# Performance work log

Measured on AMD Instinct MI355X. Metric: run time of the kernel, lower is better.

The kernel has to match this reference:

```python
import jax, jax.numpy as jnp
import numpy as np

B, S_SRC, S_TGT = 32, 128, 128
V, E, H = 32000, 256, 256
PAD_ID = 0
NEG = -1.0e9


def setup_inputs() -> dict:
    key = jax.random.key(0)
    ks = jax.random.split(key, 16)
    lengths_de = jax.random.randint(ks[0], (B,), S_SRC // 2, S_SRC + 1)
    idx_de = jax.random.randint(ks[1], (B, S_SRC), 1, V)
    pos = jnp.arange(S_SRC)[None, :]
    indices_de = jnp.where(pos < lengths_de[:, None], idx_de, PAD_ID)
    indices_en = jax.random.randint(ks[2], (B, S_TGT), 1, V)
    lengths_en = jnp.full((B,), S_TGT, dtype=jnp.int32)

    sc = 0.02
    def nrm(k, shape):
        return jax.random.normal(k, shape, dtype=jnp.float32) * sc
    emb_enc = nrm(ks[3], (V, E)).at[PAD_ID].set(0.0)
    emb_dec = nrm(ks[4], (V, E)).at[PAD_ID].set(0.0)
    return {
        "indices_de": indices_de, "lengths_de": lengths_de,
        "indices_en": indices_en, "lengths_en": lengths_en,
        "emb_enc": emb_enc, "emb_dec": emb_dec,
        "W_ih_enc": nrm(ks[5], (H, E)), "W_hh_enc": nrm(ks[6], (H, H)),
        "b_ih_enc": jnp.zeros((H,), jnp.float32), "b_hh_enc": jnp.zeros((H,), jnp.float32),
        "W_ih_dec": nrm(ks[7], (H, E)), "W_hh_dec": nrm(ks[8], (H, H)),
        "b_ih_dec": jnp.zeros((H,), jnp.float32), "b_hh_dec": jnp.zeros((H,), jnp.float32),
        "W_attn": nrm(ks[9], (H, 2 * H)), "b_attn": jnp.zeros((H,), jnp.float32),
        "W_out": nrm(ks[10], (V, H)), "b_out": jnp.zeros((V,), jnp.float32),
    }


def reference(indices_de, lengths_de, indices_en, lengths_en,
              emb_enc, emb_dec,
              W_ih_enc, W_hh_enc, b_ih_enc, b_hh_enc,
              W_ih_dec, W_hh_dec, b_ih_dec, b_hh_dec,
              W_attn, b_attn, W_out, b_out):
    # ---- Encoder: tanh RNN over packed sequence ----
    x_enc = emb_enc[indices_de]                      # [B, S, E]
    valid = jnp.arange(S_SRC)[None, :] < lengths_de[:, None]  # [B, S]

    def enc_step(h, inp):
        x_t, v_t = inp                                # [B,E], [B]
        h_new = jnp.tanh(x_t @ W_ih_enc.T + b_ih_enc + h @ W_hh_enc.T + b_hh_enc)
        h = jnp.where(v_t[:, None], h_new, h)         # frozen past length (pack semantics)
        out = jnp.where(v_t[:, None], h_new, 0.0)     # padded outputs are zero
        return h, out

    h0 = jnp.zeros((B, H), jnp.float32)
    h_final, enc_outs = jax.lax.scan(
        enc_step, h0, (x_enc.transpose(1, 0, 2), valid.T))
    encoder_outputs = enc_outs.transpose(1, 0, 2)     # [B, S, H]
    enc_mask = indices_de == PAD_ID                   # [B, S] True at padding

    # ---- Decoder: per-step RNN cell + dot-product attention + vocab proj ----
    x_dec = emb_dec[indices_en]                       # [B, T, E]

    def dec_step(h, x_t):
        h = jnp.tanh(x_t @ W_ih_dec.T + b_ih_dec + h @ W_hh_dec.T + b_hh_dec)
        scores = jnp.einsum('bh,bsh->bs', h, encoder_outputs)
        scores = jnp.where(enc_mask, NEG, scores)
        attn = jax.nn.softmax(scores, axis=-1)
        context = jnp.einsum('bs,bsh->bh', attn, encoder_outputs)
        combined = jnp.concatenate([context, h], axis=1)          # [B, 2H]
        attn_out = jnp.tanh(combined @ W_attn.T + b_attn)         # [B, H]
        logits_t = attn_out @ W_out.T + b_out                     # [B, V]
        return h, logits_t

    _, logits = jax.lax.scan(dec_step, h_final, x_dec.transpose(1, 0, 2))
    return logits.transpose(1, 0, 2)                  # [B, T, V]
```

## Files before the change

### kernel.cpp

```cpp
#include <hip/hip_runtime.h>
#include <stdint.h>

#define B_ 32
#define S_ 128
#define T_ 128
#define V_ 32000
#define E_ 256
#define H_ 256
#define NEG_ (-1.0e9f)

typedef __attribute__((ext_vector_type(8))) short short8;
typedef __attribute__((ext_vector_type(4))) float floatx4;

__device__ __forceinline__ unsigned short f2bf(float x){
  unsigned u = __float_as_uint(x);
  u = u + 0x7fffu + ((u >> 16) & 1u);
  return (unsigned short)(u >> 16);
}
__device__ __forceinline__ float bf2f(unsigned short s){
  return __uint_as_float(((unsigned)s) << 16);
}
__device__ __forceinline__ float hsum4(float4 v){ return (v.x+v.y)+(v.z+v.w); }
__device__ __forceinline__ void unpack8(uint4 q, float4& lo, float4& hi){
  lo.x = __uint_as_float(q.x << 16); lo.y = __uint_as_float(q.x & 0xffff0000u);
  lo.z = __uint_as_float(q.y << 16); lo.w = __uint_as_float(q.y & 0xffff0000u);
  hi.x = __uint_as_float(q.z << 16); hi.y = __uint_as_float(q.z & 0xffff0000u);
  hi.z = __uint_as_float(q.w << 16); hi.w = __uint_as_float(q.w & 0xffff0000u);
}

__global__ void k_cvt(const float* __restrict__ src, unsigned short* __restrict__ dst, int n4){
  int i = blockIdx.x*256 + threadIdx.x;
  if (i < n4){
    float4 v = ((const float4*)src)[i];
    ushort4 o; o.x=f2bf(v.x); o.y=f2bf(v.y); o.z=f2bf(v.z); o.w=f2bf(v.w);
    ((ushort4*)dst)[i] = o;
  }
}

__global__ __launch_bounds__(256) void k_xih(
    const int* __restrict__ idxmat,
    const float* __restrict__ emb,
    const float* __restrict__ Wih,
    const float* __restrict__ b1, const float* __restrict__ b2,
    float* __restrict__ out)
{
  __shared__ int idx_s[16];
  __shared__ float4 x_s[16][64];
  int b = blockIdx.x >> 3;
  int t0 = (blockIdx.x & 7) << 4;
  int tid = threadIdx.x;
  if (tid < 16) idx_s[tid] = idxmat[b*128 + t0 + tid];
  __syncthreads();
  for (int r = 0; r < 16; ++r)
    ((float*)&x_s[r][0])[tid] = emb[(size_t)idx_s[r]*E_ + tid];
  __syncthreads();
  int j2 = tid & 127, tg = tid >> 7;
  const float4* W0 = (const float4*)(Wih + (size_t)j2*E_);
  const float4* W1 = (const float4*)(Wih + (size_t)(j2+128)*E_);
  float4 a0[8], a1[8];
  #pragma unroll
  for (int t=0;t<8;++t){ a0[t]={0,0,0,0}; a1[t]={0,0,0,0}; }
  for (int e4 = 0; e4 < 64; ++e4){
    float4 w0 = W0[e4], w1 = W1[e4];
    #pragma unroll
    for (int t = 0; t < 8; ++t){
      float4 xv = x_s[tg*8+t][e4];
      a0[t] += w0*xv; a1[t] += w1*xv;
    }
  }
  float bi0 = b1[j2] + b2[j2];
  float bi1 = b1[j2+128] + b2[j2+128];
  #pragma unroll
  for (int t = 0; t < 8; ++t){
    size_t row = (size_t)((b<<7) + t0 + tg*8 + t)*H_;
    out[row + j2]     = hsum4(a0[t]) + bi0;
    out[row + j2+128] = hsum4(a1[t]) + bi1;
  }
}

template<int ENC>
__global__ __launch_bounds__(512, 2) void k_rnn(
    const float* __restrict__ Whh,
    const float* __restrict__ Xih,
    const float* __restrict__ h0,
    const int* __restrict__ lengths,
    unsigned short* __restrict__ enc_out,
    float* __restrict__ hseq,
    float* __restrict__ hfinal)
{
  __shared__ float4 h4_s[64];
  __shared__ float part[2][256];
  float* h_s = (float*)h4_s;
  int b = blockIdx.x, tid = threadIdx.x;
  int j = tid & 255, half = tid >> 8;
  float4 w[32];
  const float4* Wr = (const float4*)(Whh + (size_t)j*H_ + half*128);
  #pragma unroll
  for (int i = 0; i < 32; ++i) w[i] = Wr[i];
  if (tid < 256) h_s[tid] = ENC ? 0.f : h0[b*H_ + tid];
  int len = ENC ? lengths[b] : T_;
  __syncthreads();
  for (int t = 0; t < 128; ++t){
    float x = 0.f;
    if (tid < 256) x = Xih[(size_t)((b<<7) + t)*H_ + j];
    const float4* hh = h4_s + (half << 5);
    float4 acc0 = {0,0,0,0}, acc1 = {0,0,0,0};
    #pragma unroll
    for (int i = 0; i < 32; i += 2){ acc0 += w[i]*hh[i]; acc1 += w[i+1]*hh[i+1]; }
    part[half][j] = hsum4(acc0) + hsum4(acc1);
    __syncthreads();
    if (tid < 256){
      float s = x + part[0][tid] + part[1][tid];
      float hn = tanhf(s);
      if (ENC){
        float hold = h_s[tid];
        bool v = (t < len);
        h_s[tid] = v ? hn : hold;
        enc_out[(size_t)((b<<7)+t)*H_ + tid] = f2bf(v ? hn : 0.f);
      } else {
        h_s[tid] = hn;
        hseq[(size_t)((b<<7)+t)*H_ + tid] = hn;
      }
    }
    __syncthreads();
  }
  if (ENC && tid < 256) hfinal[b*H_ + tid] = h_s[tid];
}

__global__ __launch_bounds__(256) void k_attn(
    const unsigned short* __restrict__ enc_out,
    const float* __restrict__ hseq,
    const int* __restrict__ lengths,
    const unsigned short* __restrict__ Wattn,
    const float* __restrict__ battn,
    unsigned short* __restrict__ attn_out)
{
  __shared__ float h_sm[16][256];
  __shared__ float sc[16][132];
  __shared__ float comb[16][512];
  int bx = blockIdx.x; int b = bx >> 3; int t0 = (bx & 7) << 4;
  int tid = threadIdx.x;
  int len = lengths[b];
  for (int r = 0; r < 16; ++r)
    h_sm[r][tid] = hseq[(size_t)((b<<7) + t0 + r)*H_ + tid];
  __syncthreads();
  {
    int s = tid & 127, tg = tid >> 7;
    float4 a[8];
    #pragma unroll
    for (int t=0;t<8;++t) a[t] = {0,0,0,0};
    const uint4* ep = (const uint4*)(enc_out + (size_t)(b*S_ + s)*H_);
    for (int oct = 0; oct < 32; ++oct){
      uint4 q = ep[oct];
      float4 elo, ehi; unpack8(q, elo, ehi);
      #pragma unroll
      for (int t = 0; t < 8; ++t){
        const float4* hp = (const float4*)&h_sm[tg*8+t][oct*8];
        a[t] += elo*hp[0] + ehi*hp[1];
      }
    }
    #pragma unroll
    for (int t = 0; t < 8; ++t)
      sc[tg*8+t][s] = (s < len) ? hsum4(a[t]) : NEG_;
  }
  __syncthreads();
  {
    int wv = tid >> 6, ln = tid & 63;
    for (int r = 0; r < 4; ++r){
      int t = r*4 + wv;
      float v0 = sc[t][ln], v1 = sc[t][ln+64];
      float m = fmaxf(v0, v1);
      #pragma unroll
      for (int off = 32; off >= 1; off >>= 1) m = fmaxf(m, __shfl_xor(m, off));
      float e0 = __expf(v0 - m), e1 = __expf(v1 - m);
      float su = e0 + e1;
      #pragma unroll
      for (int off = 32; off >= 1; off >>= 1) su += __shfl_xor(su, off);
      float inv = 1.0f / su;
      sc[t][ln] = e0*inv; sc[t][ln+64] = e1*inv;
    }
  }
  __syncthreads();
  {
    int hd = tid & 127, tg = tid >> 7;
    float c0[8], c1[8];
    #pragma unroll
    for (int t=0;t<8;++t){ c0[t]=0.f; c1[t]=0.f; }
    for (int s4 = 0; s4 < 32; ++s4){
      float ea[4], eb[4];
      #pragma unroll
      for (int i = 0; i < 4; ++i){
        const unsigned short* er = enc_out + (size_t)(b*S_ + s4*4 + i)*H_;
        ea[i] = bf2f(er[hd]); eb[i] = bf2f(er[hd+128]);
      }
      #pragma unroll
      for (int t = 0; t < 8; ++t){
        float4 av = *(const float4*)&sc[tg*8+t][s4*4];
        c0[t] += av.x*ea[0] + av.y*ea[1] + av.z*ea[2] + av.w*ea[3];
        c1[t] += av.x*eb[0] + av.y*eb[1] + av.z*eb[2] + av.w*eb[3];
      }
    }
    #pragma unroll
    for (int t = 0; t < 8; ++t){
      comb[tg*8+t][hd]     = c0[t];
      comb[tg*8+t][hd+128] = c1[t];
    }
  }
  for (int r = 0; r < 16; ++r) comb[r][256 + tid] = h_sm[r][tid];
  __syncthreads();
  {
    int j2 = tid & 127, tg = tid >> 7;
    float4 a0[8], a1[8];
    #pragma unroll
    for (int t=0;t<8;++t){ a0[t]={0,0,0,0}; a1[t]={0,0,0,0}; }
    const uint4* W0 = (const uint4*)(Wattn + (size_t)j2*512);
    const uint4* W1 = (const uint4*)(Wattn + (size_t)(j2+128)*512);
    for (int oct = 0; oct < 64; ++oct){
      float4 w0lo, w0hi, w1lo, w1hi;
      unpack8(W0[oct], w0lo, w0hi);
      unpack8(W1[oct], w1lo, w1hi);
      #pragma unroll
      for (int t = 0; t < 8; ++t){
        const float4* cp = (const float4*)&comb[tg*8+t][oct*8];
        float4 clo = cp[0], chi = cp[1];
        a0[t] += w0lo*clo + w0hi*chi;
        a1[t] += w1lo*clo + w1hi*chi;
      }
    }
    float bi0 = battn[j2], bi1 = battn[j2+128];
    #pragma unroll
    for (int t = 0; t < 8; ++t){
      size_t row = (size_t)((b<<7) + t0 + tg*8 + t)*H_;
      attn_out[row + j2]     = f2bf(tanhf(hsum4(a0[t]) + bi0));
      attn_out[row + j2+128] = f2bf(tanhf(hsum4(a1[t]) + bi1));
    }
  }
}

__global__ __launch_bounds__(256) void k_vocab(
    const unsigned short* __restrict__ A,
    const unsigned short* __restrict__ Wb,
    const float* __restrict__ bout,
    float* __restrict__ out)
{
  int nb = blockIdx.x, mb = blockIdx.y;
  int tid = threadIdx.x;
  int wv = tid >> 6, ln = tid & 63;
  int lhi = ln >> 4, llo = ln & 15;
  int mbase = mb*128 + wv*32;
  int nbase = nb*128;
  floatx4 acc[2][8];
  #pragma unroll
  for (int mt=0;mt<2;++mt)
    #pragma unroll
    for (int nt=0;nt<8;++nt) acc[mt][nt] = (floatx4){0.f,0.f,0.f,0.f};
  #pragma unroll
  for (int k0 = 0; k0 < 8; ++k0){
    short8 af[2];
    #pragma unroll
    for (int mt = 0; mt < 2; ++mt){
      int row = mbase + mt*16 + llo;
      af[mt] = *(const short8*)(A + (size_t)row*256 + k0*32 + lhi*8);
    }
    #pragma unroll
    for (int nt = 0; nt < 8; ++nt){
      int col = nbase + nt*16 + llo;
      short8 bf = *(const short8*)(Wb + (size_t)col*256 + k0*32 + lhi*8);
      acc[0][nt] = __builtin_amdgcn_mfma_f32_16x16x32_bf16(af[0], bf, acc[0][nt], 0, 0, 0);
      acc[1][nt] = __builtin_amdgcn_mfma_f32_16x16x32_bf16(af[1], bf, acc[1][nt], 0, 0, 0);
    }
  }
  #pragma unroll
  for (int nt = 0; nt < 8; ++nt){
    int col = nbase + nt*16 + llo;
    float bias = bout[col];
    #pragma unroll
    for (int mt = 0; mt < 2; ++mt){
      #pragma unroll
      for (int r = 0; r < 4; ++r){
        int row = mbase + mt*16 + lhi*4 + r;
        out[(size_t)row*V_ + col] = acc[mt][nt][r] + bias;
      }
    }
  }
}

extern "C" void kernel_launch(void* const* d_in, const int* in_sizes, int n_in,
                              void* d_out, int out_size, void* d_ws, size_t ws_size,
                              hipStream_t stream){
  const int*   indices_de = (const int*)d_in[0];
  const int*   lengths_de = (const int*)d_in[1];
  const int*   indices_en = (const int*)d_in[2];
  const float* emb_enc   = (const float*)d_in[4];
  const float* emb_dec   = (const float*)d_in[5];
  const float* W_ih_enc  = (const float*)d_in[6];
  const float* W_hh_enc  = (const float*)d_in[7];
  const float* b_ih_enc  = (const float*)d_in[8];
  const float* b_hh_enc  = (const float*)d_in[9];
  const float* W_ih_dec  = (const float*)d_in[10];
  const float* W_hh_dec  = (const float*)d_in[11];
  const float* b_ih_dec  = (const float*)d_in[12];
  const float* b_hh_dec  = (const float*)d_in[13];
  const float* W_attn    = (const float*)d_in[14];
  const float* b_attn    = (const float*)d_in[15];
  const float* W_out     = (const float*)d_in[16];
  const float* b_out     = (const float*)d_in[17];

  char* ws = (char*)d_ws;
  size_t o = 0;
  float* Xih_enc = (float*)(ws + o); o += (size_t)4096*256*4;
  float* Xih_dec = (float*)(ws + o); o += (size_t)4096*256*4;
  unsigned short* enc_bf = (unsigned short*)(ws + o); o += (size_t)4096*256*2;
  float* hfinal  = (float*)(ws + o); o += (size_t)32*256*4;
  float* hdec    = (float*)(ws + o); o += (size_t)4096*256*4;
  unsigned short* attn_o  = (unsigned short*)(ws + o); o += (size_t)4096*256*2;
  unsigned short* Wout_bf = (unsigned short*)(ws + o); o += (size_t)V_*256*2;
  unsigned short* Wattn_bf= (unsigned short*)(ws + o); o += (size_t)256*512*2;

  k_cvt<<<8000, 256, 0, stream>>>(W_out, Wout_bf, 2048000);
  k_cvt<<<128, 256, 0, stream>>>(W_attn, Wattn_bf, 32768);
  k_xih<<<256, 256, 0, stream>>>(indices_de, emb_enc, W_ih_enc, b_ih_enc, b_hh_enc, Xih_enc);
  k_xih<<<256, 256, 0, stream>>>(indices_en, emb_dec, W_ih_dec, b_ih_dec, b_hh_dec, Xih_dec);
  k_rnn<1><<<32, 512, 0, stream>>>(W_hh_enc, Xih_enc, nullptr, lengths_de, enc_bf, nullptr, hfinal);
  k_rnn<0><<<32, 512, 0, stream>>>(W_hh_dec, Xih_dec, hfinal, nullptr, nullptr, hdec, nullptr);
  k_attn<<<256, 256, 0, stream>>>(enc_bf, hdec, lengths_de, Wattn_bf, b_attn, attn_o);
  dim3 gD(250, 32);
  k_vocab<<<gD, 256, 0, stream>>>(attn_o, Wout_bf, b_out, (float*)d_out);
}
```

Before: 1.154 ms.

## Stage vocab GEMM tiles through swizzled LDS with async double-buffered loads

The vocab projection GEMM used to read A and W fragments straight from global memory, with each wave loading its own copy. It now stages 128x32 tiles of A and W into LDS with global_load_lds, double-buffered across the K loop. Waves are arranged in a 2x2 grid, each computing a 64x64 subtile, so every LDS fragment is reused across four MFMAs. An XOR swizzle is meant to avoid LDS bank conflicts. This cuts redundant global traffic, at the cost of per-iteration barriers and 32KB of shared memory per block.

```diff
diff --git a/kernel.cpp b/kernel.cpp
--- a/kernel.cpp
+++ b/kernel.cpp
@@ -27,6 +27,11 @@
   hi.x = __uint_as_float(q.z << 16); hi.y = __uint_as_float(q.z & 0xffff0000u);
   hi.z = __uint_as_float(q.w << 16); hi.w = __uint_as_float(q.w & 0xffff0000u);
 }
+
+#define GLOAD_LDS16(gptr, lptr) \
+  __builtin_amdgcn_global_load_lds( \
+      (const __attribute__((address_space(1))) unsigned int*)(const void*)(gptr), \
+      (__attribute__((address_space(3))) unsigned int*)(void*)(lptr), 16, 0, 0)
 
 __global__ void k_cvt(const float* __restrict__ src, unsigned short* __restrict__ dst, int n4){
   int i = blockIdx.x*256 + threadIdx.x;
@@ -243,46 +248,82 @@
     const float* __restrict__ bout,
     float* __restrict__ out)
 {
+  __shared__ unsigned short Asm[2][128*32];
+  __shared__ unsigned short Bsm[2][128*32];
   int nb = blockIdx.x, mb = blockIdx.y;
   int tid = threadIdx.x;
-  int wv = tid >> 6, ln = tid & 63;
-  int lhi = ln >> 4, llo = ln & 15;
-  int mbase = mb*128 + wv*32;
-  int nbase = nb*128;
-  floatx4 acc[2][8];
-  #pragma unroll
-  for (int mt=0;mt<2;++mt)
-    #pragma unroll
-    for (int nt=0;nt<8;++nt) acc[mt][nt] = (floatx4){0.f,0.f,0.f,0.f};
+  int ln  = tid & 63;
+  int wid = tid >> 6;
+  int llo = ln & 15, lhi = ln >> 4;
+  int wr = wid >> 1, wc = wid & 1;
+  int mbase = mb*128, nbase = nb*128;
+
+  int c0 = tid, c1 = tid + 256;
+  int r0 = c0 >> 2, s0 = (c0 & 3) ^ ((r0 >> 1) & 3);
+  int r1 = c1 >> 2, s1 = (c1 & 3) ^ ((r1 >> 1) & 3);
+  const unsigned short* Ag0 = A  + (size_t)(mbase + r0)*256 + s0*8;
+  const unsigned short* Ag1 = A  + (size_t)(mbase + r1)*256 + s1*8;
+  const unsigned short* Bg0 = Wb + (size_t)(nbase + r0)*256 + s0*8;
+  const unsigned short* Bg1 = Wb + (size_t)(nbase + r1)*256 + s1*8;
+
+#define STAGE_V(bufi, kk) do { \
+    GLOAD_LDS16(Ag0 + (kk), &Asm[bufi][c0*8]); \
+    GLOAD_LDS16(Ag1 + (kk), &Asm[bufi][c1*8]); \
+    GLOAD_LDS16(Bg0 + (kk), &Bsm[bufi][c0*8]); \
+    GLOAD_LDS16(Bg1 + (kk), &Bsm[bufi][c1*8]); \
+  } while(0)
+
+  floatx4 acc[4][4];
+  #pragma unroll
+  for (int mi=0;mi<4;++mi)
+    #pragma unroll
+    for (int ni=0;ni<4;++ni) acc[mi][ni] = (floatx4){0.f,0.f,0.f,0.f};
+
+  int q = (llo >> 1) & 3;
+  int aoff[4], boff[4];
+  #pragma unroll
+  for (int i=0;i<4;++i){
+    int arow = wr*64 + i*16 + llo;
+    aoff[i] = arow*32 + ((lhi ^ q)*8);
+    int brow = wc*64 + i*16 + llo;
+    boff[i] = brow*32 + ((lhi ^ q)*8);
+  }
+
+  STAGE_V(0, 0);
+  __syncthreads();
+
   #pragma unroll
   for (int k0 = 0; k0 < 8; ++k0){
-    short8 af[2];
-    #pragma unroll
-    for (int mt = 0; mt < 2; ++mt){
-      int row = mbase + mt*16 + llo;
-      af[mt] = *(const short8*)(A + (size_t)row*256 + k0*32 + lhi*8);
-    }
-    #pragma unroll
-    for (int nt = 0; nt < 8; ++nt){
-      int col = nbase + nt*16 + llo;
-      short8 bf = *(const short8*)(Wb + (size_t)col*256 + k0*32 + lhi*8);
-      acc[0][nt] = __builtin_amdgcn_mfma_f32_16x16x32_bf16(af[0], bf, acc[0][nt], 0, 0, 0);
-      acc[1][nt] = __builtin_amdgcn_mfma_f32_16x16x32_bf16(af[1], bf, acc[1][nt], 0, 0, 0);
-    }
-  }
-  #pragma unroll
-  for (int nt = 0; nt < 8; ++nt){
-    int col = nbase + nt*16 + llo;
+    int cur = k0 & 1;
+    if (k0 < 7) STAGE_V(cur^1, (k0+1)*32);
+    short8 afr[4];
+    #pragma unroll
+    for (int mi=0;mi<4;++mi)
+      afr[mi] = *(const short8*)&Asm[cur][aoff[mi]];
+    #pragma unroll
+    for (int ni=0;ni<4;++ni){
+      short8 bfr = *(const short8*)&Bsm[cur][boff[ni]];
+      #pragma unroll
+      for (int mi=0;mi<4;++mi)
+        acc[mi][ni] = __builtin_amdgcn_mfma_f32_16x16x32_bf16(afr[mi], bfr, acc[mi][ni], 0, 0, 0);
+    }
+    __syncthreads();
+  }
+
+  #pragma unroll
+  for (int ni = 0; ni < 4; ++ni){
+    int col = nbase + wc*64 + ni*16 + llo;
     float bias = bout[col];
     #pragma unroll
-    for (int mt = 0; mt < 2; ++mt){
+    for (int mi = 0; mi < 4; ++mi){
       #pragma unroll
       for (int r = 0; r < 4; ++r){
-        int row = mbase + mt*16 + lhi*4 + r;
-        out[(size_t)row*V_ + col] = acc[mt][nt][r] + bias;
-      }
-    }
-  }
+        int row = mbase + wr*64 + mi*16 + lhi*4 + r;
+        out[(size_t)row*V_ + col] = acc[mi][ni][r] + bias;
+      }
+    }
+  }
+#undef STAGE_V
 }
 
 extern "C" void kernel_launch(void* const* d_in, const int* in_sizes, int n_in,
```

Result: faster. 995.0 us (-13.8%).
